# Performance work log

Hardware: AMD Instinct MI355X
Metric: run time of the kernel (lower is better)

Reference implementation:

```python
import jax, jax.numpy as jnp
import numpy as np

N_USERS = 100000
N_ITEMS = 100000
N = N_USERS + N_ITEMS
E = 3200000
TXT = 768
GREC = 16
D = 32            # embedding_dim (hardcoded 32 in the torch module)
LAYERS = 3        # len(weight_size)


def setup_inputs() -> dict:
    key = jax.random.key(0)
    ks = jax.random.split(key, 20)
    inp = {}
    inp["edge_row"] = jax.random.randint(ks[0], (E,), 0, N, dtype=jnp.int32)
    inp["edge_col"] = jax.random.randint(ks[1], (E,), 0, N, dtype=jnp.int32)
    # normalized adjacency values (positive, small)
    inp["adj_vals"] = jax.random.uniform(ks[2], (E,), dtype=jnp.float32) * 0.1
    inp["user_name_embs"] = jax.random.normal(ks[3], (N_USERS, TXT), dtype=jnp.float32)
    inp["sent_embs"] = jax.random.normal(ks[4], (N_ITEMS, TXT), dtype=jnp.float32)
    # learned params
    inp["user_emb"] = jax.random.normal(ks[5], (N_USERS, GREC), dtype=jnp.float32) * 0.1
    inp["item_emb"] = jax.random.normal(ks[6], (N_ITEMS, GREC), dtype=jnp.float32) * 0.1
    inp["ue_W1"] = jax.random.normal(ks[7], (TXT, 32), dtype=jnp.float32) * 0.05
    inp["ue_W2"] = jax.random.normal(ks[8], (32, GREC), dtype=jnp.float32) * 0.05
    inp["ie_W1"] = jax.random.normal(ks[9], (TXT, 32), dtype=jnp.float32) * 0.05
    inp["ie_W2"] = jax.random.normal(ks[10], (32, GREC), dtype=jnp.float32) * 0.05
    inp["gc_W"] = jax.random.normal(ks[11], (LAYERS, D, D), dtype=jnp.float32) * 0.1
    inp["gc_b"] = jnp.zeros((LAYERS, D), dtype=jnp.float32)
    inp["bi_W"] = jax.random.normal(ks[12], (LAYERS, D, D), dtype=jnp.float32) * 0.1
    inp["bi_b"] = jnp.zeros((LAYERS, D), dtype=jnp.float32)
    return inp


def _ngcf_forward(edge_row, edge_col, adj_vals, user_name_embs, sent_embs,
                  user_emb, item_emb, ue_W1, ue_W2, ie_W1, ie_W2,
                  gc_W, gc_b, bi_W, bi_b):
    # text encoders (Dropout is identity in eval mode)
    u_created = jax.nn.relu(user_name_embs @ ue_W1) @ ue_W2   # [Nu, 16]
    i_created = jax.nn.relu(sent_embs @ ie_W1) @ ie_W2         # [Ni, 16]
    agg_user = jnp.concatenate([user_emb, u_created], axis=1)  # [Nu, 32]
    agg_item = jnp.concatenate([item_emb, i_created], axis=1)  # [Ni, 32]
    ego = jnp.concatenate([agg_user, agg_item], axis=0)        # [N, 32]

    all_embeddings = [ego]
    for l in range(LAYERS):
        # sparse.mm(adj, ego): gather source rows, scale by edge value, scatter-add
        gathered = adj_vals[:, None] * ego[edge_col]           # [E, 32]
        side = jax.ops.segment_sum(gathered, edge_row, num_segments=N)  # [N, 32]
        sum_emb = jax.nn.leaky_relu(side @ gc_W[l] + gc_b[l])
        bi_emb = jax.nn.leaky_relu((ego * side) @ bi_W[l] + bi_b[l])
        ego = sum_emb + bi_emb                                 # dropout = identity (eval)
        norm = ego / jnp.maximum(
            jnp.linalg.norm(ego, axis=1, keepdims=True), 1e-12)
        all_embeddings.append(norm)
    return jnp.concatenate(all_embeddings, axis=1)             # [N, 32*(LAYERS+1)]


def reference(edge_row, edge_col, adj_vals, user_name_embs, sent_embs,
              user_emb, item_emb, ue_W1, ue_W2, ie_W1, ie_W2,
              gc_W, gc_b, bi_W, bi_b):
    all_e = _ngcf_forward(edge_row, edge_col, adj_vals, user_name_embs, sent_embs,
                          user_emb, item_emb, ue_W1, ue_W2, ie_W1, ie_W2,
                          gc_W, gc_b, bi_W, bi_b)
    u_g = all_e[:N_USERS]
    i_g = all_e[N_USERS:]
    return (u_g, i_g)
```

## Files before the change

### kernel.cpp

```cpp
#include <hip/hip_runtime.h>
#include <cstdint>

#define NU 100000
#define NI 100000
#define NN 200000
#define NE 3200000
#define TXT 768
#define NRANGE 8
#define ROWS_PER_RANGE (NN / NRANGE)
#define NBJ 313

typedef _Float16 f16x8 __attribute__((ext_vector_type(8)));
typedef _Float16 f16x4 __attribute__((ext_vector_type(4)));
typedef float    f32x4 __attribute__((ext_vector_type(4)));

typedef __attribute__((address_space(1))) const unsigned int guint;
typedef __attribute__((address_space(3))) unsigned int luint;

__device__ __forceinline__ float lrelu(float x) { return x >= 0.f ? x : 0.01f * x; }

#define MEMFENCE asm volatile("" ::: "memory")
#define WAIT_VM(N)  asm volatile("s_waitcnt vmcnt(" #N ")" ::: "memory")
#define WAIT_LGKM0  asm volatile("s_waitcnt lgkmcnt(0)" ::: "memory")
#define BARRIER     do { __builtin_amdgcn_s_barrier(); MEMFENCE; } while (0)

__global__ __launch_bounds__(256) void prep_kernel(
    const int* __restrict__ erow,
    const float* __restrict__ uemb, const float* __restrict__ iemb,
    const float* __restrict__ ueW1, const float* __restrict__ ieW1,
    int* __restrict__ cnt,
    _Float16* __restrict__ ego16, float* __restrict__ outp,
    _Float16* __restrict__ w1p)
{
    const int b = blockIdx.x;
    const int tid = threadIdx.x;

    if (b < 2504) {
        const int rlo = (b & 7) * ROWS_PER_RANGE;
        const int rhi = rlo + ROWS_PER_RANGE;
        const int bj  = b >> 3;
        const int4* e4 = (const int4*)erow;
        for (int c = bj * 256 + tid; c < NE / 4; c += NBJ * 256) {
            int4 v = e4[c];
            if (v.x >= rlo && v.x < rhi) atomicAdd(&cnt[v.x], 1);
            if (v.y >= rlo && v.y < rhi) atomicAdd(&cnt[v.y], 1);
            if (v.z >= rlo && v.z < rhi) atomicAdd(&cnt[v.z], 1);
            if (v.w >= rlo && v.w < rhi) atomicAdd(&cnt[v.w], 1);
        }
    } else if (b < 2504 + 3125) {
        int idx = (b - 2504) * 256 + tid;
        if (idx >= NN * 4) return;
        int n = idx >> 2, q = idx & 3;
        float4 v;
        if (n < NU) v = ((const float4*)uemb)[(size_t)n * 4 + q];
        else        v = ((const float4*)iemb)[(size_t)(n - NU) * 4 + q];
        f16x4 h;
        h[0] = (_Float16)v.x; h[1] = (_Float16)v.y;
        h[2] = (_Float16)v.z; h[3] = (_Float16)v.w;
        *(f16x4*)(ego16 + (size_t)n * 32 + q * 4) = h;
        ((float4*)outp)[(size_t)n * 32 + q] = v;
    } else {
        int i = (b - 5629) * 256 + tid;
        int side = (i >= 24576);
        int ii = i - side * 24576;
        const float* W1 = side ? ieW1 : ueW1;
        int j   = ii & 7;
        int ln  = (ii >> 3) & 63;
        int kbH = ii >> 9;
        int kb  = kbH >> 1, H = kbH & 1;
        int k   = kb * 32 + (ln >> 4) * 8 + j;
        int c   = H * 16 + (ln & 15);
        w1p[i] = (_Float16)W1[k * 32 + c];
    }
}

__global__ __launch_bounds__(256, 4) void mlp_mfma_v4(
    const float* __restrict__ Xu, const float* __restrict__ Xi,
    const _Float16* __restrict__ w1pack,
    const float* __restrict__ ueW2, const float* __restrict__ ieW2,
    _Float16* __restrict__ ego16,
    float* __restrict__ outp)
{
    __shared__ float buf[2][4096];
    __shared__ float part[3][512];
    __shared__ _Float16 hbuf[640];

    const int tid   = threadIdx.x;
    const int lane  = tid & 63;
    const int wv    = tid >> 6;
    const int row16 = lane & 15;
    const int cg    = lane >> 4;
    const int rx7   = row16 & 7;

    f16x8 bw2u, bw2i;
    #pragma unroll
    for (int j = 0; j < 8; ++j) {
        bw2u[j] = (_Float16)ueW2[((lane >> 4) * 8 + j) * 16 + (lane & 15)];
        bw2i[j] = (_Float16)ieW2[((lane >> 4) * 8 + j) * 16 + (lane & 15)];
    }

    const int tA = (int)(((long)blockIdx.x * 12500) >> 10);
    const int tB = (int)(((long)(blockIdx.x + 1) * 12500) >> 10);

    for (int t = tA; t < tB; ++t) {
        const bool isU = t < 6250;
        const int tile = isU ? t : t - 6250;
        const float* xt = (isU ? Xu : Xi) + (size_t)tile * 16 * TXT;
        const _Float16* w1p = w1pack + (isU ? 0 : 24576);

#define STAGE(bb, cc) do {                                                      \
            _Pragma("unroll")                                                   \
            for (int i_ = 0; i_ < 4; ++i_) {                                    \
                const int r_ = wv * 4 + i_;                                     \
                const float* g_ = xt + (size_t)r_ * TXT + (cc) * 256            \
                                  + ((lane ^ (r_ & 7)) << 2);                   \
                __builtin_amdgcn_global_load_lds((guint*)g_,                    \
                    (luint*)&buf[bb][r_ * 256], 16, 0, 0);                      \
            }                                                                   \
        } while (0)

#define MCHUNK(bb, cc) do {                                                     \
            _Pragma("unroll")                                                   \
            for (int kl2 = 0; kl2 < 2; ++kl2) {                                 \
                const int kbl = wv * 2 + kl2;                                   \
                const int kb  = (cc) * 8 + kbl;                                 \
                f16x8 b0 = *(const f16x8*)&w1p[(kb * 2 + 0) * 512 + lane * 8];  \
                f16x8 b1 = *(const f16x8*)&w1p[(kb * 2 + 1) * 512 + lane * 8];  \
                const int u0 = kbl * 8 + cg * 2;                                \
                f32x4 xa = *(const f32x4*)&buf[bb][row16 * 256 + ((u0 ^ rx7) << 2)]; \
                f32x4 xb = *(const f32x4*)&buf[bb][row16 * 256 + (((u0 + 1) ^ rx7) << 2)]; \
                f16x8 a;                                                        \
                a[0] = (_Float16)xa[0]; a[1] = (_Float16)xa[1];                 \
                a[2] = (_Float16)xa[2]; a[3] = (_Float16)xa[3];                 \
                a[4] = (_Float16)xb[0]; a[5] = (_Float16)xb[1];                 \
                a[6] = (_Float16)xb[2]; a[7] = (_Float16)xb[3];                 \
                c0 = __builtin_amdgcn_mfma_f32_16x16x32_f16(a, b0, c0, 0, 0, 0); \
                c1 = __builtin_amdgcn_mfma_f32_16x16x32_f16(a, b1, c1, 0, 0, 0); \
            }                                                                   \
        } while (0)

        f32x4 c0 = {0.f, 0.f, 0.f, 0.f};
        f32x4 c1 = {0.f, 0.f, 0.f, 0.f};

        STAGE(0, 0);
        STAGE(1, 1);
        WAIT_VM(4);
        BARRIER;
        MCHUNK(0, 0);
        WAIT_LGKM0;
        BARRIER;
        STAGE(0, 2);
        WAIT_VM(4);
        BARRIER;
        MCHUNK(1, 1);
        WAIT_LGKM0;
        WAIT_VM(0);
        BARRIER;
        MCHUNK(0, 2);
        WAIT_LGKM0;

        if (wv > 0) {
            *(f32x4*)&part[wv - 1][lane * 8]     = c0;
            *(f32x4*)&part[wv - 1][lane * 8 + 4] = c1;
            WAIT_LGKM0;
        }
        BARRIER;

        if (wv == 0) {
            #pragma unroll
            for (int p = 0; p < 3; ++p) {
                f32x4 pa = *(const f32x4*)&part[p][lane * 8];
                f32x4 pb = *(const f32x4*)&part[p][lane * 8 + 4];
                c0 += pa; c1 += pb;
            }
            #pragma unroll
            for (int j = 0; j < 4; ++j) {
                int r = cg * 4 + j;
                hbuf[r * 40 + row16]      = (_Float16)fmaxf(c0[j], 0.f);
                hbuf[r * 40 + row16 + 16] = (_Float16)fmaxf(c1[j], 0.f);
            }
            const _Float16* ap = &hbuf[row16 * 40 + cg * 8];
            f16x4 lo = *(const f16x4*)ap;
            f16x4 hi = *(const f16x4*)(ap + 4);
            f16x8 a2;
            a2[0] = lo[0]; a2[1] = lo[1]; a2[2] = lo[2]; a2[3] = lo[3];
            a2[4] = hi[0]; a2[5] = hi[1]; a2[6] = hi[2]; a2[7] = hi[3];

            f32x4 c2 = {0.f, 0.f, 0.f, 0.f};
            f16x8 bw2 = isU ? bw2u : bw2i;
            c2 = __builtin_amdgcn_mfma_f32_16x16x32_f16(a2, bw2, c2, 0, 0, 0);

            const int rbase = (isU ? 0 : NU) + tile * 16 + cg * 4;
            #pragma unroll
            for (int j = 0; j < 4; ++j) {
                float v = c2[j];
                ego16[(size_t)(rbase + j) * 32  + 16 + row16] = (_Float16)v;
                outp [(size_t)(rbase + j) * 128 + 16 + row16] = v;
            }
        }
#undef STAGE
#undef MCHUNK
    }
}

__global__ __launch_bounds__(256) void scan_blk_kernel(const int* __restrict__ cnt,
                                                       int* __restrict__ rp,
                                                       int* __restrict__ bsum)
{
    __shared__ int ts[256];
    const int tid = threadIdx.x;
    const int base = blockIdx.x * 1024 + tid * 4;
    int v0 = (base + 0 < NN) ? cnt[base + 0] : 0;
    int v1 = (base + 1 < NN) ? cnt[base + 1] : 0;
    int v2 = (base + 2 < NN) ? cnt[base + 2] : 0;
    int v3 = (base + 3 < NN) ? cnt[base + 3] : 0;
    int s = v0 + v1 + v2 + v3;
    ts[tid] = s;
    __syncthreads();
    for (int off = 1; off < 256; off <<= 1) {
        int t = (tid >= off) ? ts[tid - off] : 0;
        __syncthreads();
        ts[tid] += t;
        __syncthreads();
    }
    int excl = ts[tid] - s;
    if (base + 0 < NN) rp[base + 0] = excl;
    if (base + 1 < NN) rp[base + 1] = excl + v0;
    if (base + 2 < NN) rp[base + 2] = excl + v0 + v1;
    if (base + 3 < NN) rp[base + 3] = excl + v0 + v1 + v2;
    if (tid == 255) bsum[blockIdx.x] = ts[255];
}

__global__ __launch_bounds__(256) void scan_bsum_kernel(int* __restrict__ bsum, int nblk)
{
    __shared__ int ts[256];
    const int tid = threadIdx.x;
    int v = (tid < nblk) ? bsum[tid] : 0;
    ts[tid] = v;
    __syncthreads();
    for (int off = 1; off < 256; off <<= 1) {
        int t = (tid >= off) ? ts[tid - off] : 0;
        __syncthreads();
        ts[tid] += t;
        __syncthreads();
    }
    if (tid < nblk) bsum[tid] = ts[tid] - v;
}

__global__ __launch_bounds__(256) void add_off_kernel(int* __restrict__ rp,
                                                      const int* __restrict__ bsum,
                                                      int* __restrict__ cur)
{
    int i = blockIdx.x * 256 + threadIdx.x;
    if (i < NN) {
        int v = rp[i] + bsum[i >> 10];
        rp[i] = v;
        cur[i] = v;
    }
    if (i == 0) rp[NN] = NE;
}

__global__ __launch_bounds__(256) void fill_ranged_kernel(const int* __restrict__ erow,
                                                          const int* __restrict__ ecol,
                                                          const float* __restrict__ eval,
                                                          int* __restrict__ cur,
                                                          uint2* __restrict__ recs)
{
    const int rlo = (blockIdx.x & 7) * ROWS_PER_RANGE;
    const int rhi = rlo + ROWS_PER_RANGE;
    const int bj  = blockIdx.x >> 3;
    const int4*   e4 = (const int4*)erow;
    const int4*   c4 = (const int4*)ecol;
    const float4* f4 = (const float4*)eval;
    for (int c = bj * 256 + threadIdx.x; c < NE / 4; c += NBJ * 256) {
        int4 v   = e4[c];
        int4 cc  = c4[c];
        float4 vv = f4[c];
        if (v.x >= rlo && v.x < rhi) {
            int pos = atomicAdd(&cur[v.x], 1);
            recs[pos] = make_uint2((unsigned)cc.x | ((unsigned)(v.x & 63) << 18),
                                   __float_as_uint(vv.x));
        }
        if (v.y >= rlo && v.y < rhi) {
            int pos = atomicAdd(&cur[v.y], 1);
            recs[pos] = make_uint2((unsigned)cc.y | ((unsigned)(v.y & 63) << 18),
                                   __float_as_uint(vv.y));
        }
        if (v.z >= rlo && v.z < rhi) {
            int pos = atomicAdd(&cur[v.z], 1);
            recs[pos] = make_uint2((unsigned)cc.z | ((unsigned)(v.z & 63) << 18),
                                   __float_as_uint(vv.z));
        }
        if (v.w >= rlo && v.w < rhi) {
            int pos = atomicAdd(&cur[v.w], 1);
            recs[pos] = make_uint2((unsigned)cc.w | ((unsigned)(v.w & 63) << 18),
                                   __float_as_uint(vv.w));
        }
    }
}

__global__ __launch_bounds__(256) void pull_update_v2(
    const int* __restrict__ rp, const uint2* __restrict__ recs,
    const _Float16* __restrict__ egoIn, _Float16* __restrict__ egoOut,
    float* __restrict__ outp,
    const float* __restrict__ gcW, const float* __restrict__ gcb,
    const float* __restrict__ biW, const float* __restrict__ bib, int l)
{
    __shared__ float acc[64][33];
    __shared__ float Wg[32][36];
    __shared__ float Wb[32][36];
    __shared__ float bgs[32], bbs[32];

    const int tid = threadIdx.x;
    for (int i = tid; i < 64 * 33; i += 256) ((float*)acc)[i] = 0.f;
    for (int i = tid; i < 1024; i += 256) {
        Wg[i >> 5][i & 31] = gcW[l * 1024 + i];
        Wb[i >> 5][i & 31] = biW[l * 1024 + i];
    }
    if (tid < 32) { bgs[tid] = gcb[l * 32 + tid]; bbs[tid] = bib[l * 32 + tid]; }

    const int r0 = blockIdx.x * 64;
    const int eBeg = rp[r0], eEnd = rp[r0 + 64];
    __syncthreads();

    const int cnt = eEnd - eBeg;
    const int s   = tid >> 3;
    const int q   = tid & 7;
    const int L   = (cnt + 31) >> 5;
    const int e0  = eBeg + s * L;
    const int e1  = min(e0 + L, eEnd);

    float4 a4 = make_float4(0.f, 0.f, 0.f, 0.f);
    int curRl = -1;

    auto PROC = [&](uint2 rr, f16x4 vv) {
        int rl = rr.x >> 18;
        float a = __uint_as_float(rr.y);
        if (rl != curRl) {
            if (curRl >= 0) {
                atomicAdd(&acc[curRl][q * 4 + 0], a4.x);
                atomicAdd(&acc[curRl][q * 4 + 1], a4.y);
                atomicAdd(&acc[curRl][q * 4 + 2], a4.z);
                atomicAdd(&acc[curRl][q * 4 + 3], a4.w);
            }
            a4 = make_float4(0.f, 0.f, 0.f, 0.f);
            curRl = rl;
        }
        a4.x += a * (float)vv[0];
        a4.y += a * (float)vv[1];
        a4.z += a * (float)vv[2];
        a4.w += a * (float)vv[3];
    };

    int e = e0;
    for (; e + 8 <= e1; e += 8) {
        uint2 r0r = recs[e],     r1r = recs[e + 1];
        uint2 r2r = recs[e + 2], r3r = recs[e + 3];
        uint2 r4r = recs[e + 4], r5r = recs[e + 5];
        uint2 r6r = recs[e + 6], r7r = recs[e + 7];
        f16x4 v0 = *(const f16x4*)(egoIn + (size_t)(r0r.x & 0x3FFFF) * 32 + q * 4);
        f16x4 v1 = *(const f16x4*)(egoIn + (size_t)(r1r.x & 0x3FFFF) * 32 + q * 4);
        f16x4 v2 = *(const f16x4*)(egoIn + (size_t)(r2r.x & 0x3FFFF) * 32 + q * 4);
        f16x4 v3 = *(const f16x4*)(egoIn + (size_t)(r3r.x & 0x3FFFF) * 32 + q * 4);
        f16x4 v4 = *(const f16x4*)(egoIn + (size_t)(r4r.x & 0x3FFFF) * 32 + q * 4);
        f16x4 v5 = *(const f16x4*)(egoIn + (size_t)(r5r.x & 0x3FFFF) * 32 + q * 4);
        f16x4 v6 = *(const f16x4*)(egoIn + (size_t)(r6r.x & 0x3FFFF) * 32 + q * 4);
        f16x4 v7 = *(const f16x4*)(egoIn + (size_t)(r7r.x & 0x3FFFF) * 32 + q * 4);
        PROC(r0r, v0); PROC(r1r, v1); PROC(r2r, v2); PROC(r3r, v3);
        PROC(r4r, v4); PROC(r5r, v5); PROC(r6r, v6); PROC(r7r, v7);
    }
    for (; e < e1; ++e) {
        uint2 rr = recs[e];
        f16x4 vv = *(const f16x4*)(egoIn + (size_t)(rr.x & 0x3FFFF) * 32 + q * 4);
        PROC(rr, vv);
    }
    if (curRl >= 0) {
        atomicAdd(&acc[curRl][q * 4 + 0], a4.x);
        atomicAdd(&acc[curRl][q * 4 + 1], a4.y);
        atomicAdd(&acc[curRl][q * 4 + 2], a4.z);
        atomicAdd(&acc[curRl][q * 4 + 3], a4.w);
    }
    __syncthreads();

    const int r    = tid >> 2;
    const int c    = tid & 3;
    const int node = r0 + r;
    const int j0   = c * 8;

    const _Float16* er = egoIn + (size_t)node * 32;
    f16x8 ev0 = *(const f16x8*)er;
    f16x8 ev1 = *(const f16x8*)(er + 8);
    f16x8 ev2 = *(const f16x8*)(er + 16);
    f16x8 ev3 = *(const f16x8*)(er + 24);

    float A[8], B[8];
    #pragma unroll
    for (int jj = 0; jj < 8; ++jj) { A[jj] = bgs[j0 + jj]; B[jj] = bbs[j0 + jj]; }

    #pragma unroll
    for (int kq = 0; kq < 4; ++kq) {
        #pragma unroll
        for (int kk = 0; kk < 8; ++kk) {
            const int k = kq * 8 + kk;
            float sk = acc[r][k];
            float evk = (kq == 0) ? (float)ev0[kk] : (kq == 1) ? (float)ev1[kk]
                      : (kq == 2) ? (float)ev2[kk] : (float)ev3[kk];
            float ek = sk * evk;
            f32x4 g0 = *(const f32x4*)&Wg[k][j0];
            f32x4 g1 = *(const f32x4*)&Wg[k][j0 + 4];
            f32x4 b0 = *(const f32x4*)&Wb[k][j0];
            f32x4 b1 = *(const f32x4*)&Wb[k][j0 + 4];
            A[0] += sk * g0[0]; A[1] += sk * g0[1]; A[2] += sk * g0[2]; A[3] += sk * g0[3];
            A[4] += sk * g1[0]; A[5] += sk * g1[1]; A[6] += sk * g1[2]; A[7] += sk * g1[3];
            B[0] += ek * b0[0]; B[1] += ek * b0[1]; B[2] += ek * b0[2]; B[3] += ek * b0[3];
            B[4] += ek * b1[0]; B[5] += ek * b1[1]; B[6] += ek * b1[2]; B[7] += ek * b1[3];
        }
    }

    float v[8];
    float ss = 0.f;
    #pragma unroll
    for (int jj = 0; jj < 8; ++jj) {
        float x = lrelu(A[jj]) + lrelu(B[jj]);
        v[jj] = x;
        ss += x * x;
    }
    ss += __shfl_xor(ss, 1, 64);
    ss += __shfl_xor(ss, 2, 64);
    float inv = 1.0f / fmaxf(sqrtf(ss), 1e-12f);

    f16x8 h;
    #pragma unroll
    for (int jj = 0; jj < 8; ++jj) h[jj] = (_Float16)v[jj];
    *(f16x8*)(egoOut + (size_t)node * 32 + j0) = h;

    float* op = outp + (size_t)node * 128 + (size_t)(l + 1) * 32 + j0;
    float4 o0 = make_float4(v[0] * inv, v[1] * inv, v[2] * inv, v[3] * inv);
    float4 o1 = make_float4(v[4] * inv, v[5] * inv, v[6] * inv, v[7] * inv);
    *(float4*)op       = o0;
    *(float4*)(op + 4) = o1;
}

extern "C" void kernel_launch(void* const* d_in, const int* in_sizes, int n_in,
                              void* d_out, int out_size, void* d_ws, size_t ws_size,
                              hipStream_t stream)
{
    const int*   erow = (const int*)d_in[0];
    const int*   ecol = (const int*)d_in[1];
    const float* evalp = (const float*)d_in[2];
    const float* une  = (const float*)d_in[3];
    const float* se   = (const float*)d_in[4];
    const float* uemb = (const float*)d_in[5];
    const float* iemb = (const float*)d_in[6];
    const float* ueW1 = (const float*)d_in[7];
    const float* ueW2 = (const float*)d_in[8];
    const float* ieW1 = (const float*)d_in[9];
    const float* ieW2 = (const float*)d_in[10];
    const float* gcW  = (const float*)d_in[11];
    const float* gcb  = (const float*)d_in[12];
    const float* biW  = (const float*)d_in[13];
    const float* bib  = (const float*)d_in[14];
    float* outp = (float*)d_out;

    _Float16* egoA16 = (_Float16*)d_ws;
    _Float16* egoB16 = egoA16 + (size_t)NN * 32;
    uint2* recs = (uint2*)(egoB16 + (size_t)NN * 32);
    int*   cnt  = (int*)(recs + (size_t)NE);
    int*   rp   = cnt + NN;
    int*   cur  = rp + NN + 1;
    int*   bsum = cur + NN;
    _Float16* w1pack = (_Float16*)(bsum + 256);

    const size_t need = (size_t)((char*)(w1pack + 49152) - (char*)d_ws);
    if (ws_size < need) return;

    hipMemsetAsync(cnt, 0, (size_t)NN * sizeof(int), stream);
    prep_kernel<<<5821, 256, 0, stream>>>(erow, uemb, iemb, ueW1, ieW1,
                                          cnt, egoA16, outp, w1pack);

    mlp_mfma_v4<<<1024, 256, 0, stream>>>(une, se, w1pack, ueW2, ieW2,
                                          egoA16, outp);

    const int NBLK = (NN + 1023) / 1024;
    scan_blk_kernel<<<NBLK, 256, 0, stream>>>(cnt, rp, bsum);
    scan_bsum_kernel<<<1, 256, 0, stream>>>(bsum, NBLK);
    add_off_kernel<<<(NN + 255) / 256, 256, 0, stream>>>(rp, bsum, cur);
    fill_ranged_kernel<<<NRANGE * NBJ, 256, 0, stream>>>(erow, ecol, evalp, cur, recs);

    const _Float16* egoIn = egoA16;
    _Float16* egoOut = egoB16;
    for (int l = 0; l < 3; ++l) {
        pull_update_v2<<<NN / 64, 256, 0, stream>>>(rp, recs, egoIn, egoOut, outp,
                                                    gcW, gcb, biW, bib, l);
        const _Float16* t = egoOut; egoOut = (_Float16*)egoIn; egoIn = t;
    }
}
```

Before: 698.2 us.

## Stage edge records through LDS in chunks and reorder MLP launch after CSR build

The pull kernel now loads 2048 edge records per chunk cooperatively and coalesced into shared memory, then each 8-thread group processes a contiguous 64-record slice of that chunk, instead of each group reading its own strided slice of records from global memory. Padding records use local row 63 with zero weight so the tail is harmless. The text-encoder MLP launch also moves after the CSR construction kernels. This is meant to cut uncoalesced record loads, at the cost of extra LDS use and two block barriers per chunk.

```diff
diff --git a/kernel.cpp b/kernel.cpp
--- a/kernel.cpp
+++ b/kernel.cpp
@@ -299,7 +299,7 @@
     }
 }
 
-__global__ __launch_bounds__(256) void pull_update_v2(
+__global__ __launch_bounds__(256) void pull_update_v3(
     const int* __restrict__ rp, const uint2* __restrict__ recs,
     const _Float16* __restrict__ egoIn, _Float16* __restrict__ egoOut,
     float* __restrict__ outp,
@@ -310,6 +310,7 @@
     __shared__ float Wg[32][36];
     __shared__ float Wb[32][36];
     __shared__ float bgs[32], bbs[32];
+    __shared__ uint2 rstage[32 * 65];
 
     const int tid = threadIdx.x;
     for (int i = tid; i < 64 * 33; i += 256) ((float*)acc)[i] = 0.f;
@@ -321,14 +322,9 @@
 
     const int r0 = blockIdx.x * 64;
     const int eBeg = rp[r0], eEnd = rp[r0 + 64];
-    __syncthreads();
-
-    const int cnt = eEnd - eBeg;
-    const int s   = tid >> 3;
-    const int q   = tid & 7;
-    const int L   = (cnt + 31) >> 5;
-    const int e0  = eBeg + s * L;
-    const int e1  = min(e0 + L, eEnd);
+
+    const int s = tid >> 3;
+    const int q = tid & 7;
 
     float4 a4 = make_float4(0.f, 0.f, 0.f, 0.f);
     int curRl = -1;
@@ -352,27 +348,35 @@
         a4.w += a * (float)vv[3];
     };
 
-    int e = e0;
-    for (; e + 8 <= e1; e += 8) {
-        uint2 r0r = recs[e],     r1r = recs[e + 1];
-        uint2 r2r = recs[e + 2], r3r = recs[e + 3];
-        uint2 r4r = recs[e + 4], r5r = recs[e + 5];
-        uint2 r6r = recs[e + 6], r7r = recs[e + 7];
-        f16x4 v0 = *(const f16x4*)(egoIn + (size_t)(r0r.x & 0x3FFFF) * 32 + q * 4);
-        f16x4 v1 = *(const f16x4*)(egoIn + (size_t)(r1r.x & 0x3FFFF) * 32 + q * 4);
-        f16x4 v2 = *(const f16x4*)(egoIn + (size_t)(r2r.x & 0x3FFFF) * 32 + q * 4);
-        f16x4 v3 = *(const f16x4*)(egoIn + (size_t)(r3r.x & 0x3FFFF) * 32 + q * 4);
-        f16x4 v4 = *(const f16x4*)(egoIn + (size_t)(r4r.x & 0x3FFFF) * 32 + q * 4);
-        f16x4 v5 = *(const f16x4*)(egoIn + (size_t)(r5r.x & 0x3FFFF) * 32 + q * 4);
-        f16x4 v6 = *(const f16x4*)(egoIn + (size_t)(r6r.x & 0x3FFFF) * 32 + q * 4);
-        f16x4 v7 = *(const f16x4*)(egoIn + (size_t)(r7r.x & 0x3FFFF) * 32 + q * 4);
-        PROC(r0r, v0); PROC(r1r, v1); PROC(r2r, v2); PROC(r3r, v3);
-        PROC(r4r, v4); PROC(r5r, v5); PROC(r6r, v6); PROC(r7r, v7);
-    }
-    for (; e < e1; ++e) {
-        uint2 rr = recs[e];
-        f16x4 vv = *(const f16x4*)(egoIn + (size_t)(rr.x & 0x3FFFF) * 32 + q * 4);
-        PROC(rr, vv);
+    __syncthreads();
+
+    for (int base = eBeg; base < eEnd; base += 2048) {
+        #pragma unroll
+        for (int c = 0; c < 8; ++c) {
+            int jj = c * 256 + tid;
+            int e  = base + jj;
+            uint2 r = (e < eEnd) ? recs[e] : make_uint2(63u << 18, 0u);
+            rstage[(jj >> 6) * 65 + (jj & 63)] = r;
+        }
+        __syncthreads();
+
+        const uint2* rs = &rstage[s * 65];
+        #pragma unroll 2
+        for (int g = 0; g < 8; ++g) {
+            uint2 r0r = rs[g*8+0], r1r = rs[g*8+1], r2r = rs[g*8+2], r3r = rs[g*8+3];
+            uint2 r4r = rs[g*8+4], r5r = rs[g*8+5], r6r = rs[g*8+6], r7r = rs[g*8+7];
+            f16x4 v0 = *(const f16x4*)(egoIn + (size_t)(r0r.x & 0x3FFFF) * 32 + q * 4);
+            f16x4 v1 = *(const f16x4*)(egoIn + (size_t)(r1r.x & 0x3FFFF) * 32 + q * 4);
+            f16x4 v2 = *(const f16x4*)(egoIn + (size_t)(r2r.x & 0x3FFFF) * 32 + q * 4);
+            f16x4 v3 = *(const f16x4*)(egoIn + (size_t)(r3r.x & 0x3FFFF) * 32 + q * 4);
+            f16x4 v4 = *(const f16x4*)(egoIn + (size_t)(r4r.x & 0x3FFFF) * 32 + q * 4);
+            f16x4 v5 = *(const f16x4*)(egoIn + (size_t)(r5r.x & 0x3FFFF) * 32 + q * 4);
+            f16x4 v6 = *(const f16x4*)(egoIn + (size_t)(r6r.x & 0x3FFFF) * 32 + q * 4);
+            f16x4 v7 = *(const f16x4*)(egoIn + (size_t)(r7r.x & 0x3FFFF) * 32 + q * 4);
+            PROC(r0r, v0); PROC(r1r, v1); PROC(r2r, v2); PROC(r3r, v3);
+            PROC(r4r, v4); PROC(r5r, v5); PROC(r6r, v6); PROC(r7r, v7);
+        }
+        __syncthreads();
     }
     if (curRl >= 0) {
         atomicAdd(&acc[curRl][q * 4 + 0], a4.x);
@@ -478,19 +482,19 @@
     prep_kernel<<<5821, 256, 0, stream>>>(erow, uemb, iemb, ueW1, ieW1,
                                           cnt, egoA16, outp, w1pack);
 
-    mlp_mfma_v4<<<1024, 256, 0, stream>>>(une, se, w1pack, ueW2, ieW2,
-                                          egoA16, outp);
-
     const int NBLK = (NN + 1023) / 1024;
     scan_blk_kernel<<<NBLK, 256, 0, stream>>>(cnt, rp, bsum);
     scan_bsum_kernel<<<1, 256, 0, stream>>>(bsum, NBLK);
     add_off_kernel<<<(NN + 255) / 256, 256, 0, stream>>>(rp, bsum, cur);
     fill_ranged_kernel<<<NRANGE * NBJ, 256, 0, stream>>>(erow, ecol, evalp, cur, recs);
 
+    mlp_mfma_v4<<<1024, 256, 0, stream>>>(une, se, w1pack, ueW2, ieW2,
+                                          egoA16, outp);
+
     const _Float16* egoIn = egoA16;
     _Float16* egoOut = egoB16;
     for (int l = 0; l < 3; ++l) {
-        pull_update_v2<<<NN / 64, 256, 0, stream>>>(rp, recs, egoIn, egoOut, outp,
+        pull_update_v3<<<NN / 64, 256, 0, stream>>>(rp, recs, egoIn, egoOut, outp,
                                                     gcW, gcb, biW, bib, l);
         const _Float16* t = egoOut; egoOut = (_Float16*)egoIn; egoIn = t;
     }
```

Measured after the change: 756.4 us. 8.3% more time.
